# Kernel optimization log

Hardware: AMD Instinct MI355X
Metric: run time of the kernel (lower is better)

The kernel has to match this reference:

```python
import jax, jax.numpy as jnp
import numpy as np

N = 50000       # nodes
E = 800000      # edges
F_IN = 128      # num_node_features
H = 128         # hidden_channels
C = 10          # num_classes
G = 512         # graphs in batch


def _glorot(key, shape):
    fan_in, fan_out = shape
    lim = float(np.sqrt(6.0 / (fan_in + fan_out)))
    return jax.random.uniform(key, shape, jnp.float32, -lim, lim)


def setup_inputs() -> dict:
    key = jax.random.key(0)
    ks = jax.random.split(key, 12)
    x = jax.random.normal(ks[0], (N, F_IN), jnp.float32)
    edge_index = jax.random.randint(ks[1], (2, E), 0, N, dtype=jnp.int32).astype(jnp.int64)
    batch = jnp.sort(jax.random.randint(ks[2], (N,), 0, G, dtype=jnp.int32)).astype(jnp.int64)
    return {
        "x": x,
        "edge_index": edge_index,
        "batch": batch,
        "W1": _glorot(ks[3], (F_IN, H)), "b1": jnp.zeros((H,), jnp.float32),
        "W2": _glorot(ks[4], (H, H)),    "b2": jnp.zeros((H,), jnp.float32),
        "W3": _glorot(ks[5], (H, H)),    "b3": jnp.zeros((H,), jnp.float32),
        "W_lin": _glorot(ks[6], (H, C)), "b_lin": jnp.zeros((C,), jnp.float32),
    }


def _gcn_conv(h_in, W, b, src, dst, dis):
    # GCNConv: D^{-1/2} (A + I) D^{-1/2} (X W) + b  (symmetric norm, self-loops)
    h = h_in @ W                                   # [N, H]
    coef = (dis[src] * dis[dst])[:, None]          # [E, 1]
    msg = h[src] * coef                            # gather + scale
    agg = jax.ops.segment_sum(msg, dst, num_segments=N)  # scatter-add at targets
    agg = agg + h * (dis * dis)[:, None]           # self-loop term
    return agg + b


def reference(x, edge_index, batch, W1, b1, W2, b2, W3, b3, W_lin, b_lin):
    src, dst = edge_index[0], edge_index[1]
    # degree with self-loops (counted at aggregation target, PyG convention)
    deg = jax.ops.segment_sum(jnp.ones((E,), jnp.float32), dst, num_segments=N) + 1.0
    dis = jax.lax.rsqrt(deg)

    h = jax.nn.relu(_gcn_conv(x, W1, b1, src, dst, dis))
    h = jax.nn.relu(_gcn_conv(h, W2, b2, src, dst, dis))
    h = _gcn_conv(h, W3, b3, src, dst, dis)

    # global mean pool over graphs
    counts = jax.ops.segment_sum(jnp.ones((N,), jnp.float32), batch, num_segments=G)
    pooled = jax.ops.segment_sum(h, batch, num_segments=G)
    pooled = pooled / jnp.maximum(counts, 1.0)[:, None]

    # dropout(p=0.5, training=False) -> identity
    return pooled @ W_lin + b_lin
```

## Files before the change

kernel.cpp:

```cpp
#include <hip/hip_runtime.h>

#define NN 50000
#define NE 800000
#define FD 128
#define NG 512
#define NC 10

#define NBUCK 196
#define BSHIFT 8
#define BSTRIDE 5120
#define P1_EPB 4096
#define P1_BLOCKS ((NE + P1_EPB - 1) / P1_EPB)

typedef __attribute__((ext_vector_type(8))) short bf16x8;
typedef __attribute__((ext_vector_type(4))) float f32x4;


__device__ __forceinline__ unsigned short f2bf(float f) {
  unsigned int b = __float_as_uint(f);
  b += 0x7FFF + ((b >> 16) & 1);
  return (unsigned short)(b >> 16);
}
__device__ __forceinline__ float blo(unsigned int u) {
  return __uint_as_float(u << 16);
}
__device__ __forceinline__ float bhi(unsigned int u) {
  return __uint_as_float(u & 0xFFFF0000u);
}


__global__ __launch_bounds__(256) void setup_kernel(const float* __restrict__ W1,
                                                    const float* __restrict__ W2,
                                                    const float* __restrict__ W3,
                                                    unsigned short* __restrict__ wf1,
                                                    unsigned short* __restrict__ wf2,
                                                    unsigned short* __restrict__ wf3,
                                                    int* __restrict__ gcursor) {
  int idx = blockIdx.x * 256 + threadIdx.x;
  if (idx < 3 * 16384) {
    int wi = idx >> 14;
    int i = idx & 16383;
    const float* W = (wi == 0) ? W1 : (wi == 1) ? W2 : W3;
    unsigned short* wf = (wi == 0) ? wf1 : (wi == 1) ? wf2 : wf3;
    int j = i & 7, l = (i >> 3) & 63, ks = (i >> 9) & 3, ct = i >> 11;
    int k = ks * 32 + (l >> 4) * 8 + j;
    int c = ct * 16 + (l & 15);
    float w = W[k * 128 + c];
    unsigned int bb = __float_as_uint(w);
    unsigned int bh = bb & 0xFFFF0000u;
    float r = w - __uint_as_float(bh);
    int base = (((ct * 4 + ks) * 2 + 0) * 64 + l) * 8 + j;
    wf[base] = (unsigned short)(bh >> 16);
    wf[base + 512] = f2bf(r);
  } else {
    int t = idx - 3 * 16384;
    if (t < NBUCK) gcursor[t] = t * BSTRIDE;
  }
}
#define SETUP_BLOCKS ((3 * 16384 + NBUCK + 255) / 256)

__global__ __launch_bounds__(1024) void pass1_kernel(const int* __restrict__ ei,
                                                     int* __restrict__ gcursor,
                                                     unsigned int* __restrict__ bucketBuf) {
  __shared__ int bh[NBUCK];
  __shared__ int gbase[NBUCK];
  __shared__ int bcur[NBUCK];

  int tid = threadIdx.x;
  int e0 = blockIdx.x * P1_EPB;
  int ne = NE - e0; if (ne > P1_EPB) ne = P1_EPB;

  if (tid < NBUCK) bh[tid] = 0;
  __syncthreads();

  for (int i = tid; i < ne; i += 1024) {
    int d = ei[NE + e0 + i];
    atomicAdd(&bh[d >> BSHIFT], 1);
  }
  __syncthreads();

  if (tid < NBUCK) {
    bcur[tid] = 0;
    gbase[tid] = (bh[tid] > 0) ? atomicAdd(&gcursor[tid], bh[tid]) : 0;
  }
  __syncthreads();

  for (int i = tid; i < ne; i += 1024) {
    int s = ei[e0 + i];
    int d = ei[NE + e0 + i];
    int b = d >> BSHIFT;
    int p = atomicAdd(&bcur[b], 1);
    bucketBuf[gbase[b] + p] = (unsigned int)s | ((unsigned int)d << 16);
  }
}

__global__ __launch_bounds__(1024) void pass2_kernel(const unsigned int* __restrict__ bucketBuf,
                                                     const int* __restrict__ gcur,
                                                     int* __restrict__ offs,
                                                     float* __restrict__ dis,
                                                     unsigned short* __restrict__ csr) {
  __shared__ unsigned int raw[BSTRIDE];
  __shared__ unsigned short sorted[BSTRIDE];
  __shared__ int h[256], pos[256], cur[256];
  __shared__ int sarr[256];

  int b = blockIdx.x;
  int tid = threadIdx.x;
  int nStart = b << BSHIFT;

  if (tid < 256) sarr[tid] = (tid < NBUCK) ? (gcur[tid] - tid * BSTRIDE) : 0;
  __syncthreads();
  #pragma unroll
  for (int off = 1; off < 256; off <<= 1) {
    int v = 0;
    if (tid < 256 && tid >= off) v = sarr[tid - off];
    __syncthreads();
    if (tid < 256) sarr[tid] += v;
    __syncthreads();
  }
  int cntb = gcur[b] - b * BSTRIDE;
  int cnt = (cntb > BSTRIDE) ? BSTRIDE : cntb;
  int eStart = sarr[b] - cntb;
  if (b == NBUCK - 1 && tid == 0) offs[NN] = sarr[NBUCK - 1];

  for (int i = tid; i < cnt; i += 1024) raw[i] = bucketBuf[(size_t)b * BSTRIDE + i];
  if (tid < 256) h[tid] = 0;
  __syncthreads();

  for (int i = tid; i < cnt; i += 1024) atomicAdd(&h[(raw[i] >> 16) - nStart], 1);
  __syncthreads();

  if (tid < 256) pos[tid] = h[tid];
  __syncthreads();
  #pragma unroll
  for (int off = 1; off < 256; off <<= 1) {
    int v = 0;
    if (tid < 256 && tid >= off) v = pos[tid - off];
    __syncthreads();
    if (tid < 256) pos[tid] += v;
    __syncthreads();
  }
  if (tid < 256) {
    int ex = pos[tid] - h[tid];
    cur[tid] = ex;
    int n = nStart + tid;
    if (n < NN) {
      offs[n] = eStart + ex;
      dis[n] = rsqrtf((float)h[tid] + 1.0f);
    }
  }
  __syncthreads();

  for (int i = tid; i < cnt; i += 1024) {
    unsigned int r = raw[i];
    int d = (int)(r >> 16) - nStart;
    int p = atomicAdd(&cur[d], 1);
    sorted[p] = (unsigned short)(r & 0xFFFFu);
  }
  __syncthreads();

  for (int i = tid; i < cnt; i += 1024) csr[eStart + i] = sorted[i];
}


__global__ __launch_bounds__(256) void gemm_f32_kernel(const float* __restrict__ A,
                                                       const unsigned short* __restrict__ wf,
                                                       const float* __restrict__ dis,
                                                       unsigned short* __restrict__ Hs) {
  __shared__ unsigned short ldsW[32768];
  int tid = threadIdx.x;
  {
    const uint4* src = reinterpret_cast<const uint4*>(wf);
    uint4* dst = reinterpret_cast<uint4*>(ldsW);
    #pragma unroll
    for (int i = 0; i < 16; ++i) dst[tid + i * 256] = src[tid + i * 256];
  }
  __syncthreads();

  int w = tid >> 6, lane = tid & 63;
  int rowbase = blockIdx.x * 128 + w * 32;
  int kgrp = lane >> 4;
  int r0 = rowbase + (lane & 15);
  int r1 = r0 + 16;
  int a0 = (r0 < NN) ? r0 : 0;
  int a1 = (r1 < NN) ? r1 : 0;

  f32x4 acc0[8], acc1[8];
  #pragma unroll
  for (int ct = 0; ct < 8; ++ct) {
    f32x4 z = {0.f, 0.f, 0.f, 0.f};
    acc0[ct] = z; acc1[ct] = z;
  }

  #pragma unroll
  for (int ks = 0; ks < 4; ++ks) {
    bf16x8 ahi0, alo0, ahi1, alo1;
    {
      const float* ap = A + (size_t)a0 * FD + ks * 32 + kgrp * 8;
      float4 v0 = *reinterpret_cast<const float4*>(ap);
      float4 v1 = *reinterpret_cast<const float4*>(ap + 4);
      float a[8] = {v0.x, v0.y, v0.z, v0.w, v1.x, v1.y, v1.z, v1.w};
      #pragma unroll
      for (int j = 0; j < 8; ++j) {
        unsigned int bb = __float_as_uint(a[j]);
        unsigned int bh = bb & 0xFFFF0000u;
        float r = a[j] - __uint_as_float(bh);
        ahi0[j] = (short)(bh >> 16);
        alo0[j] = (short)f2bf(r);
      }
    }
    {
      const float* ap = A + (size_t)a1 * FD + ks * 32 + kgrp * 8;
      float4 v0 = *reinterpret_cast<const float4*>(ap);
      float4 v1 = *reinterpret_cast<const float4*>(ap + 4);
      float a[8] = {v0.x, v0.y, v0.z, v0.w, v1.x, v1.y, v1.z, v1.w};
      #pragma unroll
      for (int j = 0; j < 8; ++j) {
        unsigned int bb = __float_as_uint(a[j]);
        unsigned int bh = bb & 0xFFFF0000u;
        float r = a[j] - __uint_as_float(bh);
        ahi1[j] = (short)(bh >> 16);
        alo1[j] = (short)f2bf(r);
      }
    }
    #pragma unroll
    for (int ct = 0; ct < 8; ++ct) {
      int off = (((ct * 4 + ks) * 2) * 64 + lane) * 8;
      bf16x8 bhiV = *reinterpret_cast<const bf16x8*>(&ldsW[off]);
      bf16x8 bloV = *reinterpret_cast<const bf16x8*>(&ldsW[off + 512]);
      acc0[ct] = __builtin_amdgcn_mfma_f32_16x16x32_bf16(ahi0, bhiV, acc0[ct], 0, 0, 0);
      acc1[ct] = __builtin_amdgcn_mfma_f32_16x16x32_bf16(ahi1, bhiV, acc1[ct], 0, 0, 0);
      acc0[ct] = __builtin_amdgcn_mfma_f32_16x16x32_bf16(alo0, bhiV, acc0[ct], 0, 0, 0);
      acc1[ct] = __builtin_amdgcn_mfma_f32_16x16x32_bf16(alo1, bhiV, acc1[ct], 0, 0, 0);
      acc0[ct] = __builtin_amdgcn_mfma_f32_16x16x32_bf16(ahi0, bloV, acc0[ct], 0, 0, 0);
      acc1[ct] = __builtin_amdgcn_mfma_f32_16x16x32_bf16(ahi1, bloV, acc1[ct], 0, 0, 0);
    }
  }

  int ccol = lane & 15;
  #pragma unroll
  for (int g = 0; g < 2; ++g) {
    int crow0 = rowbase + g * 16 + kgrp * 4;
    #pragma unroll
    for (int i = 0; i < 4; ++i) {
      int r = crow0 + i;
      if (r < NN) {
        float dv = dis[r];
        #pragma unroll
        for (int ct = 0; ct < 8; ++ct) {
          float v = g ? acc1[ct][i] : acc0[ct][i];
          Hs[(size_t)r * FD + ct * 16 + ccol] = f2bf(dv * v);
        }
      }
    }
  }
}


__global__ __launch_bounds__(256) void gemm_bf16_kernel(const unsigned short* __restrict__ Ab,
                                                        const unsigned short* __restrict__ wf,
                                                        const float* __restrict__ dis,
                                                        unsigned short* __restrict__ Hs) {
  __shared__ unsigned short ldsW[32768];
  int tid = threadIdx.x;
  {
    const uint4* src = reinterpret_cast<const uint4*>(wf);
    uint4* dst = reinterpret_cast<uint4*>(ldsW);
    #pragma unroll
    for (int i = 0; i < 16; ++i) dst[tid + i * 256] = src[tid + i * 256];
  }
  __syncthreads();

  int w = tid >> 6, lane = tid & 63;
  int rowbase = blockIdx.x * 128 + w * 32;
  int kgrp = lane >> 4;
  int r0 = rowbase + (lane & 15);
  int r1 = r0 + 16;
  int a0 = (r0 < NN) ? r0 : 0;
  int a1 = (r1 < NN) ? r1 : 0;

  f32x4 acc0[8], acc1[8];
  #pragma unroll
  for (int ct = 0; ct < 8; ++ct) {
    f32x4 z = {0.f, 0.f, 0.f, 0.f};
    acc0[ct] = z; acc1[ct] = z;
  }

  #pragma unroll
  for (int ks = 0; ks < 4; ++ks) {
    bf16x8 av0, av1;
    {
      uint4 u = *reinterpret_cast<const uint4*>(&Ab[(size_t)a0 * FD + ks * 32 + kgrp * 8]);
      unsigned int uu[4] = {u.x, u.y, u.z, u.w};
      #pragma unroll
      for (int p = 0; p < 4; ++p) {
        unsigned short lo16 = (unsigned short)(uu[p] & 0xFFFFu);
        unsigned short hi16 = (unsigned short)(uu[p] >> 16);
        av0[2 * p + 0] = (short)(((short)lo16 < 0) ? 0 : lo16);
        av0[2 * p + 1] = (short)(((short)hi16 < 0) ? 0 : hi16);
      }
    }
    {
      uint4 u = *reinterpret_cast<const uint4*>(&Ab[(size_t)a1 * FD + ks * 32 + kgrp * 8]);
      unsigned int uu[4] = {u.x, u.y, u.z, u.w};
      #pragma unroll
      for (int p = 0; p < 4; ++p) {
        unsigned short lo16 = (unsigned short)(uu[p] & 0xFFFFu);
        unsigned short hi16 = (unsigned short)(uu[p] >> 16);
        av1[2 * p + 0] = (short)(((short)lo16 < 0) ? 0 : lo16);
        av1[2 * p + 1] = (short)(((short)hi16 < 0) ? 0 : hi16);
      }
    }
    #pragma unroll
    for (int ct = 0; ct < 8; ++ct) {
      int off = (((ct * 4 + ks) * 2) * 64 + lane) * 8;
      bf16x8 bhiV = *reinterpret_cast<const bf16x8*>(&ldsW[off]);
      bf16x8 bloV = *reinterpret_cast<const bf16x8*>(&ldsW[off + 512]);
      acc0[ct] = __builtin_amdgcn_mfma_f32_16x16x32_bf16(av0, bhiV, acc0[ct], 0, 0, 0);
      acc1[ct] = __builtin_amdgcn_mfma_f32_16x16x32_bf16(av1, bhiV, acc1[ct], 0, 0, 0);
      acc0[ct] = __builtin_amdgcn_mfma_f32_16x16x32_bf16(av0, bloV, acc0[ct], 0, 0, 0);
      acc1[ct] = __builtin_amdgcn_mfma_f32_16x16x32_bf16(av1, bloV, acc1[ct], 0, 0, 0);
    }
  }

  int ccol = lane & 15;
  #pragma unroll
  for (int g = 0; g < 2; ++g) {
    int crow0 = rowbase + g * 16 + kgrp * 4;
    #pragma unroll
    for (int i = 0; i < 4; ++i) {
      int r = crow0 + i;
      if (r < NN) {
        float dv = dis[r];
        #pragma unroll
        for (int ct = 0; ct < 8; ++ct) {
          float v = g ? acc1[ct][i] : acc0[ct][i];
          Hs[(size_t)r * FD + ct * 16 + ccol] = f2bf(dv * v);
        }
      }
    }
  }
}


template <bool OUT32>
__global__ __launch_bounds__(256) void agg_edge_kernel(const int* __restrict__ offs,
                                                       const unsigned short* __restrict__ csr,
                                                       const float* __restrict__ dis,
                                                       const unsigned short* __restrict__ Hs,
                                                       const float* __restrict__ bias,
                                                       void* __restrict__ AGG) {
  int node = blockIdx.x * 4 + (threadIdx.x >> 6);
  if (node >= NN) return;
  node = __builtin_amdgcn_readfirstlane(node);
  int lane = threadIdx.x & 63;
  int q = lane >> 4;
  int ch = (lane & 15) * 8;
  int beg = offs[node], end = offs[node + 1];
  float disn = dis[node];

  float accP[8], accQ[8];
  #pragma unroll
  for (int k = 0; k < 8; ++k) { accP[k] = 0.f; accQ[k] = 0.f; }

  if (q == 0) {
    uint4 hn = *reinterpret_cast<const uint4*>(&Hs[(size_t)node * FD + ch]);
    accP[0] = blo(hn.x); accP[1] = bhi(hn.x);
    accP[2] = blo(hn.y); accP[3] = bhi(hn.y);
    accP[4] = blo(hn.z); accP[5] = bhi(hn.z);
    accP[6] = blo(hn.w); accP[7] = bhi(hn.w);
  }

  int last = end - 1;
  for (int j = beg; j < end; j += 16) {
    int e0 = j + q, e1 = j + q + 4, e2 = j + q + 8, e3 = j + q + 12;
    int i0 = (e0 <= last) ? e0 : last;
    int i1 = (e1 <= last) ? e1 : last;
    int i2 = (e2 <= last) ? e2 : last;
    int i3 = (e3 <= last) ? e3 : last;
    float m0 = (e0 <= last) ? 1.f : 0.f;
    float m1 = (e1 <= last) ? 1.f : 0.f;
    float m2 = (e2 <= last) ? 1.f : 0.f;
    float m3 = (e3 <= last) ? 1.f : 0.f;
    int s0 = csr[i0], s1 = csr[i1], s2 = csr[i2], s3 = csr[i3];
    uint4 h0 = *reinterpret_cast<const uint4*>(&Hs[(size_t)s0 * FD + ch]);
    uint4 h1 = *reinterpret_cast<const uint4*>(&Hs[(size_t)s1 * FD + ch]);
    uint4 h2 = *reinterpret_cast<const uint4*>(&Hs[(size_t)s2 * FD + ch]);
    uint4 h3 = *reinterpret_cast<const uint4*>(&Hs[(size_t)s3 * FD + ch]);
    accP[0] += m0 * blo(h0.x); accP[1] += m0 * bhi(h0.x);
    accP[2] += m0 * blo(h0.y); accP[3] += m0 * bhi(h0.y);
    accP[4] += m0 * blo(h0.z); accP[5] += m0 * bhi(h0.z);
    accP[6] += m0 * blo(h0.w); accP[7] += m0 * bhi(h0.w);
    accQ[0] += m1 * blo(h1.x); accQ[1] += m1 * bhi(h1.x);
    accQ[2] += m1 * blo(h1.y); accQ[3] += m1 * bhi(h1.y);
    accQ[4] += m1 * blo(h1.z); accQ[5] += m1 * bhi(h1.z);
    accQ[6] += m1 * blo(h1.w); accQ[7] += m1 * bhi(h1.w);
    accP[0] += m2 * blo(h2.x); accP[1] += m2 * bhi(h2.x);
    accP[2] += m2 * blo(h2.y); accP[3] += m2 * bhi(h2.y);
    accP[4] += m2 * blo(h2.z); accP[5] += m2 * bhi(h2.z);
    accP[6] += m2 * blo(h2.w); accP[7] += m2 * bhi(h2.w);
    accQ[0] += m3 * blo(h3.x); accQ[1] += m3 * bhi(h3.x);
    accQ[2] += m3 * blo(h3.y); accQ[3] += m3 * bhi(h3.y);
    accQ[4] += m3 * blo(h3.z); accQ[5] += m3 * bhi(h3.z);
    accQ[6] += m3 * blo(h3.w); accQ[7] += m3 * bhi(h3.w);
  }

  float outv[8];
  #pragma unroll
  for (int k = 0; k < 8; ++k) {
    float v = accP[k] + accQ[k];
    v += __shfl_xor(v, 16, 64);
    v += __shfl_xor(v, 32, 64);
    outv[k] = v;
  }

  if (q == 0) {
    float4 b0 = *reinterpret_cast<const float4*>(&bias[ch]);
    float4 b1 = *reinterpret_cast<const float4*>(&bias[ch + 4]);
    float o[8];
    o[0] = b0.x + disn * outv[0]; o[1] = b0.y + disn * outv[1];
    o[2] = b0.z + disn * outv[2]; o[3] = b0.w + disn * outv[3];
    o[4] = b1.x + disn * outv[4]; o[5] = b1.y + disn * outv[5];
    o[6] = b1.z + disn * outv[6]; o[7] = b1.w + disn * outv[7];
    if (OUT32) {
      float* dst = reinterpret_cast<float*>(AGG) + (size_t)node * FD + ch;
      *reinterpret_cast<float4*>(dst) = make_float4(o[0], o[1], o[2], o[3]);
      *reinterpret_cast<float4*>(dst + 4) = make_float4(o[4], o[5], o[6], o[7]);
    } else {
      uint4 pk;
      pk.x = (unsigned int)f2bf(o[0]) | ((unsigned int)f2bf(o[1]) << 16);
      pk.y = (unsigned int)f2bf(o[2]) | ((unsigned int)f2bf(o[3]) << 16);
      pk.z = (unsigned int)f2bf(o[4]) | ((unsigned int)f2bf(o[5]) << 16);
      pk.w = (unsigned int)f2bf(o[6]) | ((unsigned int)f2bf(o[7]) << 16);
      unsigned short* dst = reinterpret_cast<unsigned short*>(AGG) + (size_t)node * FD + ch;
      *reinterpret_cast<uint4*>(dst) = pk;
    }
  }
}


__device__ __forceinline__ int lower_bound(const int* __restrict__ b, int n, int key) {
  int lo = 0, hi = n;
  while (lo < hi) {
    int m = (lo + hi) >> 1;
    if (b[m] < key) lo = m + 1; else hi = m;
  }
  return lo;
}

__global__ __launch_bounds__(256) void pool_final_kernel(const float* __restrict__ AGG,
                                                         const int* __restrict__ batch,
                                                         const float* __restrict__ Wl,
                                                         const float* __restrict__ bl,
                                                         float* __restrict__ out) {
  int g = blockIdx.x;
  int tid = threadIdx.x;
  int lane = tid & 63, w = tid >> 6;
  int start = lower_bound(batch, NN, g);
  int end = lower_bound(batch, NN, g + 1);

  const float2* AGG2 = reinterpret_cast<const float2*>(AGG);
  float2 acc = make_float2(0.f, 0.f);
  for (int n = start + w; n < end; n += 4) {
    float2 v = AGG2[(size_t)n * 64 + lane];
    acc.x += v.x; acc.y += v.y;
  }
  __shared__ float red[4][FD];
  red[w][lane * 2 + 0] = acc.x;
  red[w][lane * 2 + 1] = acc.y;
  __syncthreads();
  if (w == 0) {
    float px = red[0][lane * 2] + red[1][lane * 2] + red[2][lane * 2] + red[3][lane * 2];
    float py = red[0][lane * 2 + 1] + red[1][lane * 2 + 1] + red[2][lane * 2 + 1] + red[3][lane * 2 + 1];
    float inv = 1.0f / fmaxf((float)(end - start), 1.0f);
    px *= inv; py *= inv;
    float pc[NC];
    #pragma unroll
    for (int c = 0; c < NC; ++c)
      pc[c] = px * Wl[(2 * lane) * NC + c] + py * Wl[(2 * lane + 1) * NC + c];
    #pragma unroll
    for (int off = 32; off > 0; off >>= 1) {
      #pragma unroll
      for (int c = 0; c < NC; ++c) pc[c] += __shfl_down(pc[c], off, 64);
    }
    if (lane == 0) {
      #pragma unroll
      for (int c = 0; c < NC; ++c) out[g * NC + c] = pc[c] + bl[c];
    }
  }
}


extern "C" void kernel_launch(void* const* d_in, const int* in_sizes, int n_in,
                              void* d_out, int out_size, void* d_ws, size_t ws_size,
                              hipStream_t stream) {
  const float* x       = (const float*)d_in[0];
  const int* ei        = (const int*)d_in[1];
  const int* batch     = (const int*)d_in[2];
  const float* W1 = (const float*)d_in[3];
  const float* b1 = (const float*)d_in[4];
  const float* W2 = (const float*)d_in[5];
  const float* b2 = (const float*)d_in[6];
  const float* W3 = (const float*)d_in[7];
  const float* b3 = (const float*)d_in[8];
  const float* Wl = (const float*)d_in[9];
  const float* bl = (const float*)d_in[10];
  float* out = (float*)d_out;

  char* ws = (char*)d_ws;
  size_t o = 0;
  auto alloc = [&](size_t bytes) {
    void* p = ws + o;
    o += bytes;
    o = (o + 255) & ~(size_t)255;
    return p;
  };
  int*   offs   = (int*)  alloc((size_t)(NN + 1) * 4);
  float* dis    = (float*)alloc((size_t)NN * 4);
  int*   gcur   = (int*)  alloc((size_t)NBUCK * 4);
  unsigned int* bucketBuf = (unsigned int*)alloc((size_t)NBUCK * BSTRIDE * 4);
  unsigned short* csr  = (unsigned short*)alloc((size_t)NE * 2);
  unsigned short* hs   = (unsigned short*)alloc((size_t)NN * FD * 2);
  unsigned short* aggb = (unsigned short*)alloc((size_t)NN * FD * 2);
  float* aggf   = (float*)alloc((size_t)NN * FD * 4);
  unsigned short* wf1 = (unsigned short*)alloc((size_t)2 * FD * FD * 2);
  unsigned short* wf2 = (unsigned short*)alloc((size_t)2 * FD * FD * 2);
  unsigned short* wf3 = (unsigned short*)alloc((size_t)2 * FD * FD * 2);

  setup_kernel<<<SETUP_BLOCKS, 256, 0, stream>>>(W1, W2, W3, wf1, wf2, wf3, gcur);
  pass1_kernel<<<P1_BLOCKS, 1024, 0, stream>>>(ei, gcur, bucketBuf);
  pass2_kernel<<<NBUCK, 1024, 0, stream>>>(bucketBuf, gcur, offs, dis, csr);

  int gemmGrid = (NN + 127) / 128;
  int nodeGrid = (NN + 3) / 4;

  gemm_f32_kernel<<<gemmGrid, 256, 0, stream>>>(x, wf1, dis, hs);
  agg_edge_kernel<false><<<nodeGrid, 256, 0, stream>>>(offs, csr, dis, hs, b1, aggb);
  gemm_bf16_kernel<<<gemmGrid, 256, 0, stream>>>(aggb, wf2, dis, hs);
  agg_edge_kernel<false><<<nodeGrid, 256, 0, stream>>>(offs, csr, dis, hs, b2, aggb);
  gemm_bf16_kernel<<<gemmGrid, 256, 0, stream>>>(aggb, wf3, dis, hs);
  agg_edge_kernel<true><<<nodeGrid, 256, 0, stream>>>(offs, csr, dis, hs, b3, aggf);

  pool_final_kernel<<<NG, 256, 0, stream>>>(aggf, batch, Wl, bl, out);
}
```

Baseline: 172.2 us.

## Process two nodes per wavefront in edge aggregation and store final layer bf16

Each wavefront in the aggregation kernel now handles two adjacent nodes. A joint unmasked loop issues eight row gathers per iteration, and masked tail loops finish whatever edges remain for each node. The aim is more memory-level parallelism per wave and less masking overhead. The last layer's output is now written in bf16 instead of fp32, and the pooling kernel reads bf16, which halves that write and read traffic at some cost in precision. The CSR buffer gets padding, and masked-off lanes now load index 0 instead of the last edge.

```diff
diff --git a/kernel.cpp b/kernel.cpp
--- a/kernel.cpp
+++ b/kernel.cpp
@@ -343,98 +343,123 @@
 }
 
 
-template <bool OUT32>
+#define EDGE8(acc, h)                                        \
+  acc[0] += blo(h.x); acc[1] += bhi(h.x);                    \
+  acc[2] += blo(h.y); acc[3] += bhi(h.y);                    \
+  acc[4] += blo(h.z); acc[5] += bhi(h.z);                    \
+  acc[6] += blo(h.w); acc[7] += bhi(h.w);
+
+#define EDGE8M(acc, h, m)                                    \
+  acc[0] += m * blo(h.x); acc[1] += m * bhi(h.x);            \
+  acc[2] += m * blo(h.y); acc[3] += m * bhi(h.y);            \
+  acc[4] += m * blo(h.z); acc[5] += m * bhi(h.z);            \
+  acc[6] += m * blo(h.w); acc[7] += m * bhi(h.w);
+
 __global__ __launch_bounds__(256) void agg_edge_kernel(const int* __restrict__ offs,
                                                        const unsigned short* __restrict__ csr,
                                                        const float* __restrict__ dis,
                                                        const unsigned short* __restrict__ Hs,
                                                        const float* __restrict__ bias,
-                                                       void* __restrict__ AGG) {
-  int node = blockIdx.x * 4 + (threadIdx.x >> 6);
-  if (node >= NN) return;
-  node = __builtin_amdgcn_readfirstlane(node);
+                                                       unsigned short* __restrict__ AGG) {
+  int pair = blockIdx.x * 4 + (threadIdx.x >> 6);
+  int n0 = pair * 2;
+  if (n0 >= NN) return;
+  n0 = __builtin_amdgcn_readfirstlane(n0);
+  int n1 = n0 + 1;
   int lane = threadIdx.x & 63;
   int q = lane >> 4;
   int ch = (lane & 15) * 8;
-  int beg = offs[node], end = offs[node + 1];
-  float disn = dis[node];
-
-  float accP[8], accQ[8];
-  #pragma unroll
-  for (int k = 0; k < 8; ++k) { accP[k] = 0.f; accQ[k] = 0.f; }
+
+  int beg0 = offs[n0], end0 = offs[n0 + 1];
+  int beg1 = end0,     end1 = offs[n1 + 1];
+
+  float a0[8], a1[8];
+  #pragma unroll
+  for (int k = 0; k < 8; ++k) { a0[k] = 0.f; a1[k] = 0.f; }
 
   if (q == 0) {
-    uint4 hn = *reinterpret_cast<const uint4*>(&Hs[(size_t)node * FD + ch]);
-    accP[0] = blo(hn.x); accP[1] = bhi(hn.x);
-    accP[2] = blo(hn.y); accP[3] = bhi(hn.y);
-    accP[4] = blo(hn.z); accP[5] = bhi(hn.z);
-    accP[6] = blo(hn.w); accP[7] = bhi(hn.w);
-  }
-
-  int last = end - 1;
-  for (int j = beg; j < end; j += 16) {
-    int e0 = j + q, e1 = j + q + 4, e2 = j + q + 8, e3 = j + q + 12;
-    int i0 = (e0 <= last) ? e0 : last;
-    int i1 = (e1 <= last) ? e1 : last;
-    int i2 = (e2 <= last) ? e2 : last;
-    int i3 = (e3 <= last) ? e3 : last;
-    float m0 = (e0 <= last) ? 1.f : 0.f;
-    float m1 = (e1 <= last) ? 1.f : 0.f;
-    float m2 = (e2 <= last) ? 1.f : 0.f;
-    float m3 = (e3 <= last) ? 1.f : 0.f;
+    uint4 hn = *reinterpret_cast<const uint4*>(&Hs[(size_t)n0 * FD + ch]);
+    EDGE8(a0, hn);
+  } else if (q == 1) {
+    uint4 hn = *reinterpret_cast<const uint4*>(&Hs[(size_t)n1 * FD + ch]);
+    EDGE8(a1, hn);
+  }
+
+  int j0 = beg0, j1 = beg1;
+  int it = min((end0 - j0) >> 4, (end1 - j1) >> 4);
+  for (int t = 0; t < it; ++t) {
+    int s00 = csr[j0 + q], s01 = csr[j0 + q + 4], s02 = csr[j0 + q + 8], s03 = csr[j0 + q + 12];
+    int s10 = csr[j1 + q], s11 = csr[j1 + q + 4], s12 = csr[j1 + q + 8], s13 = csr[j1 + q + 12];
+    uint4 h00 = *reinterpret_cast<const uint4*>(&Hs[(size_t)s00 * FD + ch]);
+    uint4 h01 = *reinterpret_cast<const uint4*>(&Hs[(size_t)s01 * FD + ch]);
+    uint4 h02 = *reinterpret_cast<const uint4*>(&Hs[(size_t)s02 * FD + ch]);
+    uint4 h03 = *reinterpret_cast<const uint4*>(&Hs[(size_t)s03 * FD + ch]);
+    uint4 h10 = *reinterpret_cast<const uint4*>(&Hs[(size_t)s10 * FD + ch]);
+    uint4 h11 = *reinterpret_cast<const uint4*>(&Hs[(size_t)s11 * FD + ch]);
+    uint4 h12 = *reinterpret_cast<const uint4*>(&Hs[(size_t)s12 * FD + ch]);
+    uint4 h13 = *reinterpret_cast<const uint4*>(&Hs[(size_t)s13 * FD + ch]);
+    EDGE8(a0, h00); EDGE8(a0, h01); EDGE8(a0, h02); EDGE8(a0, h03);
+    EDGE8(a1, h10); EDGE8(a1, h11); EDGE8(a1, h12); EDGE8(a1, h13);
+    j0 += 16; j1 += 16;
+  }
+  for (; j0 < end0; j0 += 16) {
+    int last = end0 - 1;
+    int e0 = j0 + q, e1 = j0 + q + 4, e2 = j0 + q + 8, e3 = j0 + q + 12;
+    int i0 = (e0 <= last) ? e0 : 0, i1 = (e1 <= last) ? e1 : 0;
+    int i2 = (e2 <= last) ? e2 : 0, i3 = (e3 <= last) ? e3 : 0;
+    float m0 = (e0 <= last) ? 1.f : 0.f, m1 = (e1 <= last) ? 1.f : 0.f;
+    float m2 = (e2 <= last) ? 1.f : 0.f, m3 = (e3 <= last) ? 1.f : 0.f;
     int s0 = csr[i0], s1 = csr[i1], s2 = csr[i2], s3 = csr[i3];
     uint4 h0 = *reinterpret_cast<const uint4*>(&Hs[(size_t)s0 * FD + ch]);
     uint4 h1 = *reinterpret_cast<const uint4*>(&Hs[(size_t)s1 * FD + ch]);
     uint4 h2 = *reinterpret_cast<const uint4*>(&Hs[(size_t)s2 * FD + ch]);
     uint4 h3 = *reinterpret_cast<const uint4*>(&Hs[(size_t)s3 * FD + ch]);
-    accP[0] += m0 * blo(h0.x); accP[1] += m0 * bhi(h0.x);
-    accP[2] += m0 * blo(h0.y); accP[3] += m0 * bhi(h0.y);
-    accP[4] += m0 * blo(h0.z); accP[5] += m0 * bhi(h0.z);
-    accP[6] += m0 * blo(h0.w); accP[7] += m0 * bhi(h0.w);
-    accQ[0] += m1 * blo(h1.x); accQ[1] += m1 * bhi(h1.x);
-    accQ[2] += m1 * blo(h1.y); accQ[3] += m1 * bhi(h1.y);
-    accQ[4] += m1 * blo(h1.z); accQ[5] += m1 * bhi(h1.z);
-    accQ[6] += m1 * blo(h1.w); accQ[7] += m1 * bhi(h1.w);
-    accP[0] += m2 * blo(h2.x); accP[1] += m2 * bhi(h2.x);
-    accP[2] += m2 * blo(h2.y); accP[3] += m2 * bhi(h2.y);
-    accP[4] += m2 * blo(h2.z); accP[5] += m2 * bhi(h2.z);
-    accP[6] += m2 * blo(h2.w); accP[7] += m2 * bhi(h2.w);
-    accQ[0] += m3 * blo(h3.x); accQ[1] += m3 * bhi(h3.x);
-    accQ[2] += m3 * blo(h3.y); accQ[3] += m3 * bhi(h3.y);
-    accQ[4] += m3 * blo(h3.z); accQ[5] += m3 * bhi(h3.z);
-    accQ[6] += m3 * blo(h3.w); accQ[7] += m3 * bhi(h3.w);
-  }
-
-  float outv[8];
+    EDGE8M(a0, h0, m0); EDGE8M(a0, h1, m1); EDGE8M(a0, h2, m2); EDGE8M(a0, h3, m3);
+  }
+  for (; j1 < end1; j1 += 16) {
+    int last = end1 - 1;
+    int e0 = j1 + q, e1 = j1 + q + 4, e2 = j1 + q + 8, e3 = j1 + q + 12;
+    int i0 = (e0 <= last) ? e0 : 0, i1 = (e1 <= last) ? e1 : 0;
+    int i2 = (e2 <= last) ? e2 : 0, i3 = (e3 <= last) ? e3 : 0;
+    float m0 = (e0 <= last) ? 1.f : 0.f, m1 = (e1 <= last) ? 1.f : 0.f;
+    float m2 = (e2 <= last) ? 1.f : 0.f, m3 = (e3 <= last) ? 1.f : 0.f;
+    int s0 = csr[i0], s1 = csr[i1], s2 = csr[i2], s3 = csr[i3];
+    uint4 h0 = *reinterpret_cast<const uint4*>(&Hs[(size_t)s0 * FD + ch]);
+    uint4 h1 = *reinterpret_cast<const uint4*>(&Hs[(size_t)s1 * FD + ch]);
+    uint4 h2 = *reinterpret_cast<const uint4*>(&Hs[(size_t)s2 * FD + ch]);
+    uint4 h3 = *reinterpret_cast<const uint4*>(&Hs[(size_t)s3 * FD + ch]);
+    EDGE8M(a1, h0, m0); EDGE8M(a1, h1, m1); EDGE8M(a1, h2, m2); EDGE8M(a1, h3, m3);
+  }
+
   #pragma unroll
   for (int k = 0; k < 8; ++k) {
-    float v = accP[k] + accQ[k];
-    v += __shfl_xor(v, 16, 64);
-    v += __shfl_xor(v, 32, 64);
-    outv[k] = v;
-  }
-
-  if (q == 0) {
+    float v0 = a0[k];
+    v0 += __shfl_xor(v0, 16, 64);
+    v0 += __shfl_xor(v0, 32, 64);
+    a0[k] = v0;
+    float v1 = a1[k];
+    v1 += __shfl_xor(v1, 16, 64);
+    v1 += __shfl_xor(v1, 32, 64);
+    a1[k] = v1;
+  }
+
+  if (q < 2) {
+    int n = q ? n1 : n0;
+    float dn = dis[n];
+    const float* acc = q ? a1 : a0;
     float4 b0 = *reinterpret_cast<const float4*>(&bias[ch]);
     float4 b1 = *reinterpret_cast<const float4*>(&bias[ch + 4]);
     float o[8];
-    o[0] = b0.x + disn * outv[0]; o[1] = b0.y + disn * outv[1];
-    o[2] = b0.z + disn * outv[2]; o[3] = b0.w + disn * outv[3];
-    o[4] = b1.x + disn * outv[4]; o[5] = b1.y + disn * outv[5];
-    o[6] = b1.z + disn * outv[6]; o[7] = b1.w + disn * outv[7];
-    if (OUT32) {
-      float* dst = reinterpret_cast<float*>(AGG) + (size_t)node * FD + ch;
-      *reinterpret_cast<float4*>(dst) = make_float4(o[0], o[1], o[2], o[3]);
-      *reinterpret_cast<float4*>(dst + 4) = make_float4(o[4], o[5], o[6], o[7]);
-    } else {
-      uint4 pk;
-      pk.x = (unsigned int)f2bf(o[0]) | ((unsigned int)f2bf(o[1]) << 16);
-      pk.y = (unsigned int)f2bf(o[2]) | ((unsigned int)f2bf(o[3]) << 16);
-      pk.z = (unsigned int)f2bf(o[4]) | ((unsigned int)f2bf(o[5]) << 16);
-      pk.w = (unsigned int)f2bf(o[6]) | ((unsigned int)f2bf(o[7]) << 16);
-      unsigned short* dst = reinterpret_cast<unsigned short*>(AGG) + (size_t)node * FD + ch;
-      *reinterpret_cast<uint4*>(dst) = pk;
-    }
+    o[0] = b0.x + dn * acc[0]; o[1] = b0.y + dn * acc[1];
+    o[2] = b0.z + dn * acc[2]; o[3] = b0.w + dn * acc[3];
+    o[4] = b1.x + dn * acc[4]; o[5] = b1.y + dn * acc[5];
+    o[6] = b1.z + dn * acc[6]; o[7] = b1.w + dn * acc[7];
+    uint4 pk;
+    pk.x = (unsigned int)f2bf(o[0]) | ((unsigned int)f2bf(o[1]) << 16);
+    pk.y = (unsigned int)f2bf(o[2]) | ((unsigned int)f2bf(o[3]) << 16);
+    pk.z = (unsigned int)f2bf(o[4]) | ((unsigned int)f2bf(o[5]) << 16);
+    pk.w = (unsigned int)f2bf(o[6]) | ((unsigned int)f2bf(o[7]) << 16);
+    *reinterpret_cast<uint4*>(&AGG[(size_t)n * FD + ch]) = pk;
   }
 }
 
@@ -448,7 +473,7 @@
   return lo;
 }
 
-__global__ __launch_bounds__(256) void pool_final_kernel(const float* __restrict__ AGG,
+__global__ __launch_bounds__(256) void pool_final_kernel(const unsigned short* __restrict__ AGG,
                                                          const int* __restrict__ batch,
                                                          const float* __restrict__ Wl,
                                                          const float* __restrict__ bl,
@@ -459,11 +484,11 @@
   int start = lower_bound(batch, NN, g);
   int end = lower_bound(batch, NN, g + 1);
 
-  const float2* AGG2 = reinterpret_cast<const float2*>(AGG);
   float2 acc = make_float2(0.f, 0.f);
   for (int n = start + w; n < end; n += 4) {
-    float2 v = AGG2[(size_t)n * 64 + lane];
-    acc.x += v.x; acc.y += v.y;
+    unsigned int v = *reinterpret_cast<const unsigned int*>(&AGG[(size_t)n * FD + lane * 2]);
+    acc.x += blo(v);
+    acc.y += bhi(v);
   }
   __shared__ float red[4][FD];
   red[w][lane * 2 + 0] = acc.x;
@@ -519,10 +544,9 @@
   float* dis    = (float*)alloc((size_t)NN * 4);
   int*   gcur   = (int*)  alloc((size_t)NBUCK * 4);
   unsigned int* bucketBuf = (unsigned int*)alloc((size_t)NBUCK * BSTRIDE * 4);
-  unsigned short* csr  = (unsigned short*)alloc((size_t)NE * 2);
+  unsigned short* csr  = (unsigned short*)alloc((size_t)NE * 2 + 64);
   unsigned short* hs   = (unsigned short*)alloc((size_t)NN * FD * 2);
   unsigned short* aggb = (unsigned short*)alloc((size_t)NN * FD * 2);
-  float* aggf   = (float*)alloc((size_t)NN * FD * 4);
   unsigned short* wf1 = (unsigned short*)alloc((size_t)2 * FD * FD * 2);
   unsigned short* wf2 = (unsigned short*)alloc((size_t)2 * FD * FD * 2);
   unsigned short* wf3 = (unsigned short*)alloc((size_t)2 * FD * FD * 2);
@@ -532,14 +556,14 @@
   pass2_kernel<<<NBUCK, 1024, 0, stream>>>(bucketBuf, gcur, offs, dis, csr);
 
   int gemmGrid = (NN + 127) / 128;
-  int nodeGrid = (NN + 3) / 4;
+  int aggGrid = (NN / 2 + 3) / 4;
 
   gemm_f32_kernel<<<gemmGrid, 256, 0, stream>>>(x, wf1, dis, hs);
-  agg_edge_kernel<false><<<nodeGrid, 256, 0, stream>>>(offs, csr, dis, hs, b1, aggb);
+  agg_edge_kernel<<<aggGrid, 256, 0, stream>>>(offs, csr, dis, hs, b1, aggb);
   gemm_bf16_kernel<<<gemmGrid, 256, 0, stream>>>(aggb, wf2, dis, hs);
-  agg_edge_kernel<false><<<nodeGrid, 256, 0, stream>>>(offs, csr, dis, hs, b2, aggb);
+  agg_edge_kernel<<<aggGrid, 256, 0, stream>>>(offs, csr, dis, hs, b2, aggb);
   gemm_bf16_kernel<<<gemmGrid, 256, 0, stream>>>(aggb, wf3, dis, hs);
-  agg_edge_kernel<true><<<nodeGrid, 256, 0, stream>>>(offs, csr, dis, hs, b3, aggf);
-
-  pool_final_kernel<<<NG, 256, 0, stream>>>(aggf, batch, Wl, bl, out);
-}
+  agg_edge_kernel<<<aggGrid, 256, 0, stream>>>(offs, csr, dis, hs, b3, aggb);
+
+  pool_final_kernel<<<NG, 256, 0, stream>>>(aggb, batch, Wl, bl, out);
+}
```

New measurement: 171.5 us. No clear change (-0.4%).
